# Performance work log

Measured on AMD Instinct MI355X. Metric: run time of the kernel, lower is better.

## Reference

```python
import jax, jax.numpy as jnp
import numpy as np

# OGB full_atom_feature_dims
FEAT_DIMS = np.array([119, 5, 12, 12, 10, 6, 6, 2, 2], dtype=np.int32)
OFFSETS = jnp.asarray(np.concatenate([[0], np.cumsum(FEAT_DIMS)[:-1]]), dtype=jnp.int32)  # [9]
TOTAL_ROWS = int(FEAT_DIMS.sum())  # 174
DIM = 256
N_CLASS = 10
B, MAX_NODE = 128, 1024


def setup_inputs() -> dict:
    key = jax.random.key(0)
    ks = jax.random.split(key, 16)
    # per-field valid categorical indices, stacked -> [B, MAX_NODE, 9]
    cols = [jax.random.randint(ks[i], (B, MAX_NODE), 0, int(FEAT_DIMS[i]), dtype=jnp.int32)
            for i in range(9)]
    node_feat = jnp.stack(cols, axis=-1)
    num_nodes = jax.random.randint(ks[9], (B,), 1, MAX_NODE + 1, dtype=jnp.int32)
    rxn_class = jax.random.randint(ks[10], (B,), 0, N_CLASS, dtype=jnp.int32)
    # learned params
    atom_emb = jax.random.normal(ks[11], (TOTAL_ROWS, DIM), dtype=jnp.float32) * 0.02
    rxn_emb = jax.random.normal(ks[12], (N_CLASS, DIM), dtype=jnp.float32) * 0.02
    lin_w = jax.random.normal(ks[13], (DIM, 2 * DIM), dtype=jnp.float32) * (1.0 / np.sqrt(2 * DIM))
    lin_b = jax.random.normal(ks[14], (DIM,), dtype=jnp.float32) * 0.01
    return {"node_feat": node_feat, "num_nodes": num_nodes, "rxn_class": rxn_class,
            "atom_emb": atom_emb, "rxn_emb": rxn_emb, "lin_w": lin_w, "lin_b": lin_b}


def reference(node_feat, num_nodes, rxn_class, atom_emb, rxn_emb, lin_w, lin_b):
    # AtomEncoder: sum of 9 per-field embedding lookups (tables concatenated with offsets)
    idx = node_feat + OFFSETS  # [B, N, 9]
    enc = atom_emb[idx].sum(axis=2)  # [B, N, dim]
    # zero-pad positions beyond num_nodes (ragged-to-dense scatter)
    mask = (jnp.arange(MAX_NODE)[None, :] < num_nodes[:, None])[..., None]  # [B, N, 1]
    enc = jnp.where(mask, enc, jnp.zeros((), dtype=enc.dtype))
    # class embedding broadcast over all node slots (including padding, as in original)
    cls = jnp.broadcast_to(rxn_emb[rxn_class][:, None, :], enc.shape)  # [B, N, dim]
    h = jnp.concatenate([enc, cls], axis=-1)  # [B, N, 2*dim]
    out = jnp.einsum('bnd,od->bno', h, lin_w) + lin_b  # [B, N, dim]
    return out
```

## Files before the change

### kernel.cpp

```cpp
#include <hip/hip_runtime.h>
#include <stdint.h>

#define BATCH 128
#define MAXN 1024
#define NF 9
#define DIM 256
#define NCLS 10

#define BASE1 119
#define BASE2 179
#define BASE3 299
#define QROWS 443

#define TBLK 114
#define PACKBLK (BATCH * MAXN / 256)

typedef __attribute__((ext_vector_type(4))) float f32x4;
typedef __attribute__((ext_vector_type(2))) uint32_t u32x2;

__device__ __forceinline__ ushort f32_to_bf16_rne(float x) {
  uint32_t u = __float_as_uint(x);
  u += 0x7fffu + ((u >> 16) & 1u);
  return (ushort)(u >> 16);
}

__device__ __forceinline__ f32x4 bf4_to_f32x4(u32x2 v) {
  f32x4 r;
  r.x = __uint_as_float(v.x << 16);
  r.y = __uint_as_float(v.x & 0xffff0000u);
  r.z = __uint_as_float(v.y << 16);
  r.w = __uint_as_float(v.y & 0xffff0000u);
  return r;
}

__global__ __launch_bounds__(256) void prep_kernel(
    const float* __restrict__ rxn_emb, const float* __restrict__ lin_w,
    const float* __restrict__ lin_b, const float* __restrict__ atom_emb,
    const int* __restrict__ node_feat,
    ushort* __restrict__ Qb, float* __restrict__ clsT, int4* __restrict__ jpack)
{
  const int bid = blockIdx.x;
  const int t = threadIdx.x;

  if (bid >= TBLK) {
    const int node = (bid - TBLK) * 256 + t;
    const int* p = node_feat + (size_t)node * NF;
    int4 jv;
    jv.x = p[0];
    jv.y = BASE1 + p[1] * 12 + p[2];
    jv.z = BASE2 + p[3] * 10 + p[4];
    jv.w = BASE3 + ((p[5] * 6 + p[6]) * 2 + p[7]) * 2 + p[8];
    jpack[node] = jv;
    return;
  }

  __shared__ float S[4][DIM];
  const bool isCls = bid < 3;
  const int row0 = isCls ? bid * 4 : (bid - 3) * 4;
  const int rmax = isCls ? NCLS : QROWS;
  const int nrows = (rmax - row0 < 4) ? (rmax - row0) : 4;

#pragma unroll
  for (int r = 0; r < 4; ++r) {
    float v = 0.f;
    if (r < nrows) {
      const int q = row0 + r;
      if (isCls) {
        v = rxn_emb[q * DIM + t];
      } else if (q < BASE1) {
        v = atom_emb[q * DIM + t];
      } else if (q < BASE2) {
        int x = q - BASE1;
        v = atom_emb[(119 + x / 12) * DIM + t] + atom_emb[(124 + x % 12) * DIM + t];
      } else if (q < BASE3) {
        int x = q - BASE2;
        v = atom_emb[(136 + x / 10) * DIM + t] + atom_emb[(148 + x % 10) * DIM + t];
      } else {
        int x = q - BASE3;
        int i8 = x & 1, i7 = (x >> 1) & 1, y = x >> 2;
        v = atom_emb[(158 + y / 6) * DIM + t] + atom_emb[(164 + y % 6) * DIM + t]
          + atom_emb[(170 + i7) * DIM + t] + atom_emb[(172 + i8) * DIM + t];
      }
    }
    S[r][t] = v;
  }
  __syncthreads();

  const float* wrow = lin_w + (size_t)t * 2 * DIM + (isCls ? DIM : 0);
  const float init = isCls ? lin_b[t] : 0.f;
  float a0 = init, a1 = init, a2 = init, a3 = init;
#pragma unroll 4
  for (int d = 0; d < DIM; d += 4) {
    float4 w4 = *(const float4*)(wrow + d);
    a0 += w4.x * S[0][d] + w4.y * S[0][d + 1] + w4.z * S[0][d + 2] + w4.w * S[0][d + 3];
    a1 += w4.x * S[1][d] + w4.y * S[1][d + 1] + w4.z * S[1][d + 2] + w4.w * S[1][d + 3];
    a2 += w4.x * S[2][d] + w4.y * S[2][d + 1] + w4.z * S[2][d + 2] + w4.w * S[2][d + 3];
    a3 += w4.x * S[3][d] + w4.y * S[3][d + 1] + w4.z * S[3][d + 2] + w4.w * S[3][d + 3];
  }
  if (isCls) {
    if (0 < nrows) clsT[(row0 + 0) * DIM + t] = a0;
    if (1 < nrows) clsT[(row0 + 1) * DIM + t] = a1;
    if (2 < nrows) clsT[(row0 + 2) * DIM + t] = a2;
    if (3 < nrows) clsT[(row0 + 3) * DIM + t] = a3;
  } else {
    if (0 < nrows) Qb[(row0 + 0) * DIM + t] = f32_to_bf16_rne(a0);
    if (1 < nrows) Qb[(row0 + 1) * DIM + t] = f32_to_bf16_rne(a1);
    if (2 < nrows) Qb[(row0 + 2) * DIM + t] = f32_to_bf16_rne(a2);
    if (3 < nrows) Qb[(row0 + 3) * DIM + t] = f32_to_bf16_rne(a3);
  }
}

__global__ __launch_bounds__(256) void main_kernel(
    const int4* __restrict__ jpack, const int* __restrict__ num_nodes,
    const int* __restrict__ rxn_class,
    const ushort* __restrict__ Qb, const float* __restrict__ clsT,
    float* __restrict__ out)
{
  const int tid = threadIdx.x;
  const int lane = tid & 63;
  const int w = __builtin_amdgcn_readfirstlane(tid >> 6);
  const int wid = blockIdx.x * 4 + w;
  const int b = wid >> 6;
  const int n0 = (wid & 63) << 4;
  const int nn = num_nodes[b];

  const f32x4 cf = ((const f32x4*)clsT)[rxn_class[b] * 64 + lane];
  f32x4* __restrict__ outp = (f32x4*)out + ((size_t)(b * MAXN + n0)) * 64 + lane;

  if (n0 >= nn) {
#pragma unroll
    for (int i = 0; i < 16; ++i)
      outp[i * 64] = cf;
    return;
  }

  const int4* __restrict__ jp = jpack + (size_t)b * MAXN + n0;
  const u32x2* __restrict__ Q2 = (const u32x2*)Qb;

  if (n0 + 16 <= nn) {
#pragma unroll 8
    for (int i = 0; i < 16; ++i) {
      const int4 jv = jp[i];
      const u32x2 v0 = Q2[jv.x * 64 + lane];
      const u32x2 v1 = Q2[jv.y * 64 + lane];
      const u32x2 v2 = Q2[jv.z * 64 + lane];
      const u32x2 v3 = Q2[jv.w * 64 + lane];
      const f32x4 s = (bf4_to_f32x4(v0) + bf4_to_f32x4(v1))
                    + (bf4_to_f32x4(v2) + bf4_to_f32x4(v3));
      outp[i * 64] = cf + s;
    }
    return;
  }

#pragma unroll 8
  for (int i = 0; i < 16; ++i) {
    const int4 jv = jp[i];
    const u32x2 v0 = Q2[jv.x * 64 + lane];
    const u32x2 v1 = Q2[jv.y * 64 + lane];
    const u32x2 v2 = Q2[jv.z * 64 + lane];
    const u32x2 v3 = Q2[jv.w * 64 + lane];
    const float m = (n0 + i < nn) ? 1.f : 0.f;
    const f32x4 s = (bf4_to_f32x4(v0) + bf4_to_f32x4(v1))
                  + (bf4_to_f32x4(v2) + bf4_to_f32x4(v3));
    outp[i * 64] = cf + m * s;
  }
}

extern "C" void kernel_launch(void* const* d_in, const int* in_sizes, int n_in,
                              void* d_out, int out_size, void* d_ws, size_t ws_size,
                              hipStream_t stream) {
  const int* node_feat = (const int*)d_in[0];
  const int* num_nodes = (const int*)d_in[1];
  const int* rxn_class = (const int*)d_in[2];
  const float* atom_emb = (const float*)d_in[3];
  const float* rxn_emb = (const float*)d_in[4];
  const float* lin_w = (const float*)d_in[5];
  const float* lin_b = (const float*)d_in[6];
  float* outp = (float*)d_out;

  ushort* Qb = (ushort*)d_ws;
  float* clsT = (float*)((char*)d_ws + QROWS * DIM * sizeof(ushort));
  int4* jpack = (int4*)((char*)d_ws + 262144);

  prep_kernel<<<TBLK + PACKBLK, 256, 0, stream>>>(rxn_emb, lin_w, lin_b,
                                                  atom_emb, node_feat,
                                                  Qb, clsT, jpack);
  main_kernel<<<2048, 256, 0, stream>>>(jpack, num_nodes, rxn_class,
                                        Qb, clsT, outp);
}
```

Measured before the change: 44.92 us.

## Stage column-sliced bf16 lookup table in shared memory for main gather

The precomputed bf16 combination table is now stored as four 64-column slices. Each 1024-thread block copies one slice (about 57 KB) into LDS and gathers from LDS instead of global/L2. Blocks cover one batch, a quarter of the nodes and one column slice, so each output row is written in 256-byte pieces by four blocks. The goal is to cut the latency of the random global gathers. The cost is a per-block LDS fill, lower occupancy from the large LDS footprint, and less contiguous output stores.

```diff
diff --git a/kernel.cpp b/kernel.cpp
--- a/kernel.cpp
+++ b/kernel.cpp
@@ -14,6 +14,10 @@
 
 #define TBLK 114
 #define PACKBLK (BATCH * MAXN / 256)
+
+#define NSL 4
+#define SCOL 64
+#define SLICE_U4 3544
 
 typedef __attribute__((ext_vector_type(4))) float f32x4;
 typedef __attribute__((ext_vector_type(2))) uint32_t u32x2;
@@ -103,66 +107,100 @@
     if (2 < nrows) clsT[(row0 + 2) * DIM + t] = a2;
     if (3 < nrows) clsT[(row0 + 3) * DIM + t] = a3;
   } else {
-    if (0 < nrows) Qb[(row0 + 0) * DIM + t] = f32_to_bf16_rne(a0);
-    if (1 < nrows) Qb[(row0 + 1) * DIM + t] = f32_to_bf16_rne(a1);
-    if (2 < nrows) Qb[(row0 + 2) * DIM + t] = f32_to_bf16_rne(a2);
-    if (3 < nrows) Qb[(row0 + 3) * DIM + t] = f32_to_bf16_rne(a3);
-  }
-}
-
-__global__ __launch_bounds__(256) void main_kernel(
+    const int s = t >> 6, c = t & 63;
+    if (0 < nrows) Qb[(size_t)s * QROWS * SCOL + (row0 + 0) * SCOL + c] = f32_to_bf16_rne(a0);
+    if (1 < nrows) Qb[(size_t)s * QROWS * SCOL + (row0 + 1) * SCOL + c] = f32_to_bf16_rne(a1);
+    if (2 < nrows) Qb[(size_t)s * QROWS * SCOL + (row0 + 2) * SCOL + c] = f32_to_bf16_rne(a2);
+    if (3 < nrows) Qb[(size_t)s * QROWS * SCOL + (row0 + 3) * SCOL + c] = f32_to_bf16_rne(a3);
+  }
+}
+
+__global__ __launch_bounds__(1024, 8) void main_kernel(
     const int4* __restrict__ jpack, const int* __restrict__ num_nodes,
     const int* __restrict__ rxn_class,
     const ushort* __restrict__ Qb, const float* __restrict__ clsT,
     float* __restrict__ out)
 {
+  __shared__ ushort Ls[QROWS * SCOL];
+
   const int tid = threadIdx.x;
+  const int bid = blockIdx.x;
+  const int s = bid & 3;
+  const int b = (bid >> 2) & 127;
+  const int q = bid >> 9;
+  const int n0_blk = q * 256;
+  const int nn = num_nodes[b];
+  const int cls = rxn_class[b];
+  const f32x4* __restrict__ clsT4 = (const f32x4*)clsT;
+  f32x4* __restrict__ out4 = (f32x4*)out;
+
+  if (n0_blk >= nn) {
+    const f32x4 cf = clsT4[cls * 64 + s * 16 + (tid & 15)];
+    const size_t base = (size_t)(b * MAXN + n0_blk) * 64 + s * 16;
+#pragma unroll
+    for (int k = 0; k < 4; ++k) {
+      const int idx = tid + k * 1024;
+      const int node = idx >> 4, c4 = idx & 15;
+      out4[base + (size_t)node * 64 + c4] = cf;
+    }
+    return;
+  }
+
+  {
+    const uint4* __restrict__ src = (const uint4*)(Qb + (size_t)s * QROWS * SCOL);
+    uint4* dst = (uint4*)Ls;
+    for (int i = tid; i < SLICE_U4; i += 1024) dst[i] = src[i];
+  }
+  __syncthreads();
+
+  const int w = __builtin_amdgcn_readfirstlane(tid >> 6);
   const int lane = tid & 63;
-  const int w = __builtin_amdgcn_readfirstlane(tid >> 6);
-  const int wid = blockIdx.x * 4 + w;
-  const int b = wid >> 6;
-  const int n0 = (wid & 63) << 4;
-  const int nn = num_nodes[b];
-
-  const f32x4 cf = ((const f32x4*)clsT)[rxn_class[b] * 64 + lane];
-  f32x4* __restrict__ outp = (f32x4*)out + ((size_t)(b * MAXN + n0)) * 64 + lane;
+  const int nd = lane >> 4;
+  const int c = lane & 15;
+  const int n0 = n0_blk + w * 16;
+
+  const f32x4 cf = clsT4[cls * 64 + s * 16 + c];
+  const u32x2* __restrict__ L2p = (const u32x2*)Ls;
+  const int4* __restrict__ jp = jpack + (size_t)b * MAXN;
+  const size_t obase = (size_t)(b * MAXN) * 64 + s * 16 + c;
 
   if (n0 >= nn) {
 #pragma unroll
-    for (int i = 0; i < 16; ++i)
-      outp[i * 64] = cf;
-    return;
-  }
-
-  const int4* __restrict__ jp = jpack + (size_t)b * MAXN + n0;
-  const u32x2* __restrict__ Q2 = (const u32x2*)Qb;
+    for (int p = 0; p < 4; ++p) {
+      const int n = n0 + p * 4 + nd;
+      out4[obase + (size_t)n * 64] = cf;
+    }
+    return;
+  }
 
   if (n0 + 16 <= nn) {
-#pragma unroll 8
-    for (int i = 0; i < 16; ++i) {
-      const int4 jv = jp[i];
-      const u32x2 v0 = Q2[jv.x * 64 + lane];
-      const u32x2 v1 = Q2[jv.y * 64 + lane];
-      const u32x2 v2 = Q2[jv.z * 64 + lane];
-      const u32x2 v3 = Q2[jv.w * 64 + lane];
-      const f32x4 s = (bf4_to_f32x4(v0) + bf4_to_f32x4(v1))
+#pragma unroll
+    for (int p = 0; p < 4; ++p) {
+      const int n = n0 + p * 4 + nd;
+      const int4 jv = jp[n];
+      const u32x2 v0 = L2p[jv.x * 16 + c];
+      const u32x2 v1 = L2p[jv.y * 16 + c];
+      const u32x2 v2 = L2p[jv.z * 16 + c];
+      const u32x2 v3 = L2p[jv.w * 16 + c];
+      const f32x4 sum = (bf4_to_f32x4(v0) + bf4_to_f32x4(v1))
+                      + (bf4_to_f32x4(v2) + bf4_to_f32x4(v3));
+      out4[obase + (size_t)n * 64] = cf + sum;
+    }
+    return;
+  }
+
+#pragma unroll
+  for (int p = 0; p < 4; ++p) {
+    const int n = n0 + p * 4 + nd;
+    const int4 jv = jp[n];
+    const u32x2 v0 = L2p[jv.x * 16 + c];
+    const u32x2 v1 = L2p[jv.y * 16 + c];
+    const u32x2 v2 = L2p[jv.z * 16 + c];
+    const u32x2 v3 = L2p[jv.w * 16 + c];
+    const float m = (n < nn) ? 1.f : 0.f;
+    const f32x4 sum = (bf4_to_f32x4(v0) + bf4_to_f32x4(v1))
                     + (bf4_to_f32x4(v2) + bf4_to_f32x4(v3));
-      outp[i * 64] = cf + s;
-    }
-    return;
-  }
-
-#pragma unroll 8
-  for (int i = 0; i < 16; ++i) {
-    const int4 jv = jp[i];
-    const u32x2 v0 = Q2[jv.x * 64 + lane];
-    const u32x2 v1 = Q2[jv.y * 64 + lane];
-    const u32x2 v2 = Q2[jv.z * 64 + lane];
-    const u32x2 v3 = Q2[jv.w * 64 + lane];
-    const float m = (n0 + i < nn) ? 1.f : 0.f;
-    const f32x4 s = (bf4_to_f32x4(v0) + bf4_to_f32x4(v1))
-                  + (bf4_to_f32x4(v2) + bf4_to_f32x4(v3));
-    outp[i * 64] = cf + m * s;
+    out4[obase + (size_t)n * 64] = cf + m * sum;
   }
 }
 
@@ -185,6 +223,6 @@
   prep_kernel<<<TBLK + PACKBLK, 256, 0, stream>>>(rxn_emb, lin_w, lin_b,
                                                   atom_emb, node_feat,
                                                   Qb, clsT, jpack);
-  main_kernel<<<2048, 256, 0, stream>>>(jpack, num_nodes, rxn_class,
-                                        Qb, clsT, outp);
-}
+  main_kernel<<<NSL * BATCH * 4, 1024, 0, stream>>>(jpack, num_nodes, rxn_class,
+                                                    Qb, clsT, outp);
+}
```

Measured after the change: 40.86 us. 1.1x faster.
